# Kernel tuning notes

Measured on AMD Instinct MI355X. Metric: run time of the kernel, lower is better.

Reference implementation:

```python
import jax, jax.numpy as jnp
import numpy as np

B, N, M, K = 4, 16384, 16384, 16   # batch, points, centers, neighbors
C, O, G = 64, 64, 8                # in_planes, out_planes, group


def setup_inputs() -> dict:
    key = jax.random.key(0)
    ks = jax.random.split(key, 16)
    r = lambda i, sh, s=1.0: jax.random.normal(ks[i], sh, jnp.float32) * s
    return dict(
        center_pos=r(0, (B, M, 3)),
        center_fea=r(1, (B, C, M)),
        pos=r(2, (B, N, 3)),
        fea=r(3, (B, C, N)),
        idx=jax.random.randint(ks[4], (B, M, K), 0, N, jnp.int32),
        # linear q/k/v
        Wq=r(5, (C, O), 0.05), bq=jnp.zeros((O,), jnp.float32),
        Wk=r(6, (C, O), 0.05), bk=jnp.zeros((O,), jnp.float32),
        Wv=r(7, (C, O), 0.05), bv=jnp.zeros((O,), jnp.float32),
        # center_pos_encode: conv1x1(3->O, no bias) + folded BN (scale,shift) + relu + conv1x1(O->O)
        cpe_w1=r(8, (3, O), 0.05), cpe_s=jnp.ones((O,), jnp.float32), cpe_b=jnp.zeros((O,), jnp.float32),
        cpe_w2=r(9, (O, O), 0.05), cpe_b2=jnp.zeros((O,), jnp.float32),
        # pos_encode (Conv2d 1x1 == per-point linear)
        pe_w1=r(10, (3, O), 0.05), pe_s=jnp.ones((O,), jnp.float32), pe_b=jnp.zeros((O,), jnp.float32),
        pe_w2=r(11, (O, O), 0.05), pe_b2=jnp.zeros((O,), jnp.float32),
        # weight_encode (O -> G)
        we_w1=r(12, (O, G), 0.05), we_s=jnp.ones((G,), jnp.float32), we_b=jnp.zeros((G,), jnp.float32),
        we_w2=r(13, (G, G), 0.05), we_b2=jnp.zeros((G,), jnp.float32),
    )


def _mlp2(x, w1, s, b, w2, b2):
    # conv1x1(no bias) -> inference BatchNorm folded to (scale, shift) -> ReLU -> conv1x1(+bias)
    h = jax.nn.relu(x @ w1 * s + b)
    return h @ w2 + b2


def reference(center_pos, center_fea, pos, fea, idx,
              Wq, bq, Wk, bk, Wv, bv,
              cpe_w1, cpe_s, cpe_b, cpe_w2, cpe_b2,
              pe_w1, pe_s, pe_b, pe_w2, pe_b2,
              we_w1, we_s, we_b, we_w2, we_b2):
    x_q = center_fea.transpose(0, 2, 1) @ Wq + bq        # [B,M,O]
    ft = fea.transpose(0, 2, 1)                          # [B,N,C]
    x_k = ft @ Wk + bk                                   # [B,N,O]
    x_v = ft @ Wv + bv                                   # [B,N,O]

    gather = jax.vmap(lambda a, i: a[i])                 # per-batch irregular gather
    nk = gather(x_k, idx)                                # [B,M,K,O]
    nv = gather(x_v, idx)                                # [B,M,K,O]
    npos = gather(pos, idx) - center_pos[:, :, None, :]  # [B,M,K,3] relative coords

    cpr = _mlp2(center_pos, cpe_w1, cpe_s, cpe_b, cpe_w2, cpe_b2)  # [B,M,O]
    pr = _mlp2(npos, pe_w1, pe_s, pe_b, pe_w2, pe_b2)              # [B,M,K,O]

    r_qk = nk - x_q[:, :, None, :] + cpr[:, :, None, :]  # [B,M,K,O]
    v = nv + pr                                          # [B,M,K,O]

    w = _mlp2(r_qk, we_w1, we_s, we_b, we_w2, we_b2)     # [B,M,K,G]
    w = jax.nn.softmax(w, axis=2)                        # softmax over neighbors

    v = v.reshape(B, M, K, G, O // G)
    out = jnp.einsum('bmkgi,bmkg->bmgi', v, w).reshape(B, M, O)
    return out.transpose(0, 2, 1)                        # [B,O,M]
```

## Files before the change

### kernel.cpp

```cpp
#include <hip/hip_runtime.h>
#include <hip/hip_bf16.h>

typedef unsigned short u16;
typedef __attribute__((ext_vector_type(8))) __bf16 bf8v;
typedef __attribute__((ext_vector_type(4))) float f32x4;
typedef __attribute__((ext_vector_type(4))) unsigned uint4v;

#define B_ 4
#define N_ 16384
#define M_ 16384
#define K_ 16
#define C_ 64
#define O_ 64
#define G_ 8

__device__ __forceinline__ float bf2f(u16 x){
  union { unsigned u; float f; } v; v.u = ((unsigned)x) << 16; return v.f;
}
__device__ __forceinline__ u16 f2bf(float f){
  union { float f; unsigned u; } v; v.f = f;
  unsigned u = v.u;
  return (u16)((u + 0x7FFFu + ((u >> 16) & 1u)) >> 16);
}

__global__ __launch_bounds__(256) void pre_kernel(
    const float* __restrict__ center_pos, const float* __restrict__ center_fea,
    const float* __restrict__ fea,
    const float* __restrict__ Wq, const float* __restrict__ bq,
    const float* __restrict__ Wk, const float* __restrict__ bk,
    const float* __restrict__ Wv, const float* __restrict__ bv,
    const float* __restrict__ cpe_w1, const float* __restrict__ cpe_s, const float* __restrict__ cpe_b,
    const float* __restrict__ cpe_w2, const float* __restrict__ cpe_b2,
    const float* __restrict__ we_w1,
    u16* __restrict__ xk, u16* __restrict__ xv, float* __restrict__ qw)
{
  int tid = threadIdx.x;
  int blk = blockIdx.x;
  __shared__ u16 sWT[128*72];
  __shared__ u16 sOut[64*136];
  __shared__ float sMisc[784];

  int l = tid & 63, w = tid >> 6, c = l & 15, q = l >> 4;

  if (blk < 1024) {
    int P0 = blk * 64; int b = P0 >> 14; int n0 = P0 & (N_-1);
    for (int e = tid; e < 8192; e += 256){
      int k = e >> 7, col = e & 127;
      float v = (col < 64) ? Wk[k*64 + col] : Wv[k*64 + (col-64)];
      sWT[col*72 + k] = f2bf(v);
    }
    if (tid < 128) sMisc[tid] = (tid < 64) ? bk[tid] : bv[tid-64];
    __syncthreads();

    int mIdx = n0 + w*16 + c;
    const float* fb = fea + (long)b*C_*N_;
    bf8v af[2];
    #pragma unroll
    for (int ks=0; ks<2; ks++){
      union { bf8v v; u16 s[8]; } ua;
      #pragma unroll
      for (int j=0; j<8; j++)
        ua.s[j] = f2bf(fb[(long)(ks*32 + q*8 + j)*N_ + mIdx]);
      af[ks] = ua.v;
    }

    f32x4 acc[8];
    #pragma unroll
    for (int t=0; t<8; t++){
      float bias = sMisc[16*t + c];
      f32x4 a_ = {bias, bias, bias, bias};
      bf8v b0 = *(const bf8v*)&sWT[(16*t + c)*72 + q*8];
      bf8v b1 = *(const bf8v*)&sWT[(16*t + c)*72 + 32 + q*8];
      a_ = __builtin_amdgcn_mfma_f32_16x16x32_bf16(af[0], b0, a_, 0,0,0);
      a_ = __builtin_amdgcn_mfma_f32_16x16x32_bf16(af[1], b1, a_, 0,0,0);
      acc[t] = a_;
    }

    #pragma unroll
    for (int t=0; t<8; t++)
      #pragma unroll
      for (int r=0; r<4; r++)
        sOut[(w*16 + q*4 + r)*136 + 16*t + c] = f2bf(acc[t][r]);
    __syncthreads();

    #pragma unroll
    for (int rep=0; rep<4; rep++){
      int chunk = rep*256 + tid;
      int pt = chunk >> 4, c8i = chunk & 15;
      uint4v val = *(const uint4v*)&sOut[pt*136 + c8i*8];
      int col8 = c8i*8;
      long row = (long)P0 + pt;
      if (col8 < 64) *(uint4v*)(xk + row*64 + col8)      = val;
      else           *(uint4v*)(xv + row*64 + (col8-64)) = val;
    }
  } else {
    int P0 = (blk - 1024) * 64; int b = P0 >> 14; int m0 = P0 & (M_-1);
    for (int e = tid; e < 512; e += 256) sMisc[e] = we_w1[e];
    if (tid < 64){
      float sc = cpe_s[tid];
      sMisc[512+tid] = cpe_w1[tid]      * sc;
      sMisc[576+tid] = cpe_w1[64+tid]   * sc;
      sMisc[640+tid] = cpe_w1[128+tid]  * sc;
      sMisc[704+tid] = cpe_b[tid];
    }
    __syncthreads();

    {
      int k = tid >> 1, g0 = (tid & 1)*4;
      const float* brow = (k < 64) ? (cpe_w2 + k*64) : (Wq + (k-64)*64);
      float sgn = (k < 64) ? 1.f : -1.f;
      float aw[4] = {0.f,0.f,0.f,0.f};
      for (int o=0; o<64; o++){
        float bo = brow[o]*sgn;
        #pragma unroll
        for (int gg=0; gg<4; gg++) aw[gg] += bo * sMisc[o*8 + g0+gg];
      }
      #pragma unroll
      for (int gg=0; gg<4; gg++) sWT[(g0+gg)*136 + k] = f2bf(aw[gg]);
    }
    for (int e = tid; e < 1088; e += 256) sWT[1088 + e] = 0;
    if (tid < 8){
      float s = 0.f;
      for (int o=0; o<64; o++) s += (cpe_b2[o] - bq[o]) * sMisc[o*8 + tid];
      sMisc[768 + tid] = s;
    }
    __syncthreads();

    int pg = P0 + w*16 + c;
    int mIdx = m0 + w*16 + c;
    long c3 = (long)pg * 3;
    float cp0 = center_pos[c3], cp1 = center_pos[c3+1], cp2 = center_pos[c3+2];
    bf8v ah[2], acf[2];
    #pragma unroll
    for (int ks=0; ks<2; ks++){
      union { bf8v v; u16 s[8]; } ua;
      #pragma unroll
      for (int j=0; j<8; j++){
        int h = ks*32 + q*8 + j;
        float hv = cp0*sMisc[512+h] + cp1*sMisc[576+h] + cp2*sMisc[640+h] + sMisc[704+h];
        ua.s[j] = f2bf(fmaxf(hv, 0.f));
      }
      ah[ks] = ua.v;
    }
    const float* cfb = center_fea + (long)b*C_*M_;
    #pragma unroll
    for (int ks=0; ks<2; ks++){
      union { bf8v v; u16 s[8]; } ua;
      #pragma unroll
      for (int j=0; j<8; j++)
        ua.s[j] = f2bf(cfb[(long)(ks*32 + q*8 + j)*M_ + mIdx]);
      acf[ks] = ua.v;
    }

    float cinit = (c < 8) ? sMisc[768 + c] : 0.f;
    f32x4 aq = {cinit, cinit, cinit, cinit};
    {
      bf8v b0 = *(const bf8v*)&sWT[c*136 + q*8];
      bf8v b1 = *(const bf8v*)&sWT[c*136 + 32 + q*8];
      bf8v b2 = *(const bf8v*)&sWT[c*136 + 64 + q*8];
      bf8v b3 = *(const bf8v*)&sWT[c*136 + 96 + q*8];
      aq = __builtin_amdgcn_mfma_f32_16x16x32_bf16(ah[0], b0, aq, 0,0,0);
      aq = __builtin_amdgcn_mfma_f32_16x16x32_bf16(ah[1], b1, aq, 0,0,0);
      aq = __builtin_amdgcn_mfma_f32_16x16x32_bf16(acf[0], b2, aq, 0,0,0);
      aq = __builtin_amdgcn_mfma_f32_16x16x32_bf16(acf[1], b3, aq, 0,0,0);
    }
    __syncthreads();
    if (c < 8){
      #pragma unroll
      for (int r=0; r<4; r++) sMisc[(w*16 + q*4 + r)*8 + c] = aq[r];
    }
    __syncthreads();
    for (int e = tid; e < 512; e += 256)
      qw[(long)P0*8 + e] = sMisc[e];
  }
}

__global__ __launch_bounds__(256) void attn_kernel(
    const float* __restrict__ center_pos, const float* __restrict__ pos,
    const int* __restrict__ idx,
    const float* __restrict__ pe_w1, const float* __restrict__ pe_s, const float* __restrict__ pe_b,
    const float* __restrict__ pe_w2, const float* __restrict__ pe_b2,
    const float* __restrict__ we_w1, const float* __restrict__ we_s, const float* __restrict__ we_b,
    const float* __restrict__ we_w2, const float* __restrict__ we_b2,
    const u16* __restrict__ xk, const u16* __restrict__ xv, const float* __restrict__ qw,
    float* __restrict__ out)
{
  int tid = threadIdx.x;
  __shared__ float s_w1f[192];
  __shared__ float s_pb[64];
  __shared__ float s_ws[8], s_wb[8], s_wb2[8];
  __shared__ float s_ww2[64];
  __shared__ float s_pb2[64];
  __shared__ u16  s_vt[4*16*72];
  __shared__ float s_tile[32*66];

  if (tid < 64){
    float sc = pe_s[tid];
    s_w1f[tid]     = pe_w1[tid]*sc;
    s_w1f[64+tid]  = pe_w1[64+tid]*sc;
    s_w1f[128+tid] = pe_w1[128+tid]*sc;
    s_pb[tid]  = pe_b[tid];
    s_pb2[tid] = pe_b2[tid];
    s_ww2[tid] = we_w2[tid];
  }
  if (tid >= 64 && tid < 72){
    int g = tid-64;
    s_ws[g]=we_s[g]; s_wb[g]=we_b[g]; s_wb2[g]=we_b2[g];
  }
  __syncthreads();

  int w = tid >> 6, l = tid & 63, c = l & 15, q = l >> 4, c8 = c & 7, qb = l & 48;

  bf8v pw2f[4][2], ww1f[2];
  {
    union { bf8v v; u16 s[8]; } u_;
    #pragma unroll
    for (int t=0;t<4;t++)
      #pragma unroll
      for (int ks=0;ks<2;ks++){
        #pragma unroll
        for (int j=0;j<8;j++) u_.s[j] = f2bf(pe_w2[(ks*32 + q*8 + j)*64 + t*16 + c]);
        pw2f[t][ks] = u_.v;
      }
    #pragma unroll
    for (int ks=0;ks<2;ks++){
      #pragma unroll
      for (int j=0;j<8;j++) u_.s[j] = (c < 8) ? f2bf(we_w1[(ks*32 + q*8 + j)*8 + c]) : (u16)0;
      ww1f[ks] = u_.v;
    }
  }
  float ws_c = s_ws[c8], wb_c = s_wb[c8], wb2_c = s_wb2[c8];
  float w2col[8];
  #pragma unroll
  for (int g=0; g<8; g++) w2col[g] = s_ww2[g*8 + c8];
  float pb2t[4];
  #pragma unroll
  for (int t=0;t<4;t++) pb2t[t] = s_pb2[t*16 + c];

  int pbase = blockIdx.x * 32;
  int b = pbase >> 14;
  long xkb = (long)b * N_ * 64;
  u16* vt = s_vt + w*(16*72);

  int p = pbase + w*8;
  int iv = idx[(long)p*16 + c];
  float qpv = qw[(long)p*8 + c8];
  long c30 = (long)p*3;
  float cp0 = center_pos[c30], cp1 = center_pos[c30+1], cp2 = center_pos[c30+2];

  #pragma unroll 1
  for (int i = 0; i < 8; i++){
    long pr3 = ((long)b*N_ + iv) * 3;
    float np0 = pos[pr3]   - cp0;
    float np1 = pos[pr3+1] - cp1;
    float np2 = pos[pr3+2] - cp2;
    const u16* krow = xk + xkb + (long)iv * 64;
    bf8v ka0 = *(const bf8v*)(krow + q*8);
    bf8v ka1 = *(const bf8v*)(krow + 32 + q*8);
    const u16* vrow = xv + xkb + (long)iv * 64;
    uint4v va0 = *(const uint4v*)(vrow + q*8);
    uint4v va1 = *(const uint4v*)(vrow + 32 + q*8);

    int pn = p + ((i < 7) ? 1 : 0);
    int iv_n = idx[(long)pn*16 + c];
    float qpv_n = qw[(long)pn*8 + c8];
    long c3n = (long)pn*3;
    float cpn0 = center_pos[c3n], cpn1 = center_pos[c3n+1], cpn2 = center_pos[c3n+2];

    *(uint4v*)&vt[c*72 + q*8]      = va0;
    *(uint4v*)&vt[c*72 + 32 + q*8] = va1;

    bf8v h1f[2];
    {
      union { bf8v v; u16 s[8]; } hu;
      #pragma unroll
      for (int ks=0;ks<2;ks++){
        #pragma unroll
        for (int j=0;j<8;j++){
          int o = ks*32 + q*8 + j;
          float hv = np0*s_w1f[o] + np1*s_w1f[64+o] + np2*s_w1f[128+o] + s_pb[o];
          hu.s[j] = f2bf(fmaxf(hv, 0.f));
        }
        h1f[ks] = hu.v;
      }
    }

    f32x4 h2a = {qpv, qpv, qpv, qpv};
    h2a = __builtin_amdgcn_mfma_f32_16x16x32_bf16(ka0, ww1f[0], h2a, 0, 0, 0);
    h2a = __builtin_amdgcn_mfma_f32_16x16x32_bf16(ka1, ww1f[1], h2a, 0, 0, 0);

    f32x4 prA[4];
    #pragma unroll
    for (int t=0;t<4;t++){
      f32x4 z = {0.f,0.f,0.f,0.f};
      z = __builtin_amdgcn_mfma_f32_16x16x32_bf16(h1f[0], pw2f[t][0], z, 0, 0, 0);
      z = __builtin_amdgcn_mfma_f32_16x16x32_bf16(h1f[1], pw2f[t][1], z, 0, 0, 0);
      prA[t] = z;
    }

    float h2r[4];
    #pragma unroll
    for (int r=0;r<4;r++) h2r[r] = fmaxf(h2a[r]*ws_c + wb_c, 0.f);
    float wl[4] = {wb2_c, wb2_c, wb2_c, wb2_c};
    #pragma unroll
    for (int g=0; g<8; g++){
      float wg = w2col[g];
      #pragma unroll
      for (int r=0;r<4;r++)
        wl[r] += __shfl(h2r[r], qb | g, 64) * wg;
    }
    float mx = fmaxf(fmaxf(wl[0],wl[1]), fmaxf(wl[2],wl[3]));
    mx = fmaxf(mx, __shfl_xor(mx, 16, 64));
    mx = fmaxf(mx, __shfl_xor(mx, 32, 64));
    float e[4];
    #pragma unroll
    for (int r=0;r<4;r++) e[r] = exp2f((wl[r]-mx)*1.44269504f);
    float sm = e[0]+e[1]+e[2]+e[3];
    sm += __shfl_xor(sm, 16, 64);
    sm += __shfl_xor(sm, 32, 64);
    float rn = 1.0f / sm;
    #pragma unroll
    for (int r=0;r<4;r++) e[r] *= rn;

    float ov[4] = {0.f,0.f,0.f,0.f};
    int ch = c >> 3;
    #pragma unroll
    for (int r=0;r<4;r++){
      #pragma unroll
      for (int t=0;t<4;t++){
        float wv_ = __shfl(e[r], qb | (t*2 + ch), 64);
        float nvv = bf2f(vt[(q*4+r)*72 + t*16 + c]);
        ov[t] += (prA[t][r] + nvv) * wv_;
      }
    }
    #pragma unroll
    for (int t=0;t<4;t++){
      ov[t] += __shfl_xor(ov[t], 16, 64);
      ov[t] += __shfl_xor(ov[t], 32, 64);
      ov[t] += pb2t[t];
    }
    float selv = ov[0];
    selv = (q==1) ? ov[1] : selv;
    selv = (q==2) ? ov[2] : selv;
    selv = (q==3) ? ov[3] : selv;
    s_tile[(w*8+i)*66 + l] = selv;

    p = pn; iv = iv_n; qpv = qpv_n; cp0 = cpn0; cp1 = cpn1; cp2 = cpn2;
  }
  __syncthreads();

  int o0 = tid >> 5, pt = tid & 31;
  int m0 = pbase & (M_-1);
  long outb = ((long)b*64) * M_ + m0 + pt;
  #pragma unroll
  for (int ii=0; ii<8; ii++){
    int o = o0*8 + ii;
    out[outb + (long)o*M_] = s_tile[pt*66 + o];
  }
}

extern "C" void kernel_launch(void* const* d_in, const int* in_sizes, int n_in,
                              void* d_out, int out_size, void* d_ws, size_t ws_size,
                              hipStream_t stream) {
  const float* center_pos = (const float*)d_in[0];
  const float* center_fea = (const float*)d_in[1];
  const float* pos        = (const float*)d_in[2];
  const float* fea        = (const float*)d_in[3];
  const int*   idx        = (const int*)d_in[4];
  const float* Wq = (const float*)d_in[5];   const float* bq = (const float*)d_in[6];
  const float* Wk = (const float*)d_in[7];   const float* bk = (const float*)d_in[8];
  const float* Wv = (const float*)d_in[9];   const float* bv = (const float*)d_in[10];
  const float* cpe_w1 = (const float*)d_in[11]; const float* cpe_s = (const float*)d_in[12];
  const float* cpe_b  = (const float*)d_in[13]; const float* cpe_w2 = (const float*)d_in[14];
  const float* cpe_b2 = (const float*)d_in[15];
  const float* pe_w1 = (const float*)d_in[16]; const float* pe_s = (const float*)d_in[17];
  const float* pe_b  = (const float*)d_in[18]; const float* pe_w2 = (const float*)d_in[19];
  const float* pe_b2 = (const float*)d_in[20];
  const float* we_w1 = (const float*)d_in[21]; const float* we_s = (const float*)d_in[22];
  const float* we_b  = (const float*)d_in[23]; const float* we_w2 = (const float*)d_in[24];
  const float* we_b2 = (const float*)d_in[25];

  const size_t SZ = (size_t)B_*N_*64;
  u16* xk = (u16*)d_ws;
  u16* xv = xk + SZ;
  float* qwp = (float*)(xv + SZ);
  float* outp = (float*)d_out;

  hipLaunchKernelGGL(pre_kernel, dim3(2048), dim3(256), 0, stream,
      center_pos, center_fea, fea, Wq, bq, Wk, bk, Wv, bv,
      cpe_w1, cpe_s, cpe_b, cpe_w2, cpe_b2, we_w1, xk, xv, qwp);
  hipLaunchKernelGGL(attn_kernel, dim3(2048), dim3(256), 0, stream,
      center_pos, pos, idx, pe_w1, pe_s, pe_b, pe_w2, pe_b2,
      we_w1, we_s, we_b, we_w2, we_b2, xk, xv, qwp, outp);
}
```

Baseline: 225.8 us.

## Persist pre_kernel blocks over four tiles, prefetch gathers, pack softmax shuffles in fp16

pre_kernel now launches a quarter as many blocks. Each block builds its weights once, then loops over four 64-point tiles and prefetches the next tile's fea and center_fea into registers. attn_kernel prefetches the next point's pos, xk and xv rows one iteration ahead to hide gather latency. It also packs h2 and softmax weights into fp16 pairs, halving shuffle count. The softmax max-subtraction is removed, which trades numerical safety against overflow for fewer instructions, and the fp16 packing reduces precision.

```diff
diff --git a/kernel.cpp b/kernel.cpp
--- a/kernel.cpp
+++ b/kernel.cpp
@@ -21,6 +21,10 @@
   union { float f; unsigned u; } v; v.f = f;
   unsigned u = v.u;
   return (u16)((u + 0x7FFFu + ((u >> 16) & 1u)) >> 16);
+}
+union pk2 { unsigned u; _Float16 h[2]; };
+__device__ __forceinline__ unsigned packh(float a, float b){
+  pk2 p; p.h[0] = (_Float16)a; p.h[1] = (_Float16)b; return p.u;
 }
 
 __global__ __launch_bounds__(256) void pre_kernel(
@@ -42,8 +46,18 @@
 
   int l = tid & 63, w = tid >> 6, c = l & 15, q = l >> 4;
 
-  if (blk < 1024) {
-    int P0 = blk * 64; int b = P0 >> 14; int n0 = P0 & (N_-1);
+  if (blk < 256) {
+    int P0 = blk * 256; int b = P0 >> 14; int n00 = P0 & (N_-1);
+    const float* fb = fea + (long)b*C_*N_;
+
+    float ar[16];
+    {
+      int mI = n00 + w*16 + c;
+      #pragma unroll
+      for (int e=0; e<16; e++)
+        ar[e] = fb[(long)((e>>3)*32 + q*8 + (e&7))*N_ + mI];
+    }
+
     for (int e = tid; e < 8192; e += 256){
       int k = e >> 7, col = e & 127;
       float v = (col < 64) ? Wk[k*64 + col] : Wv[k*64 + (col-64)];
@@ -52,49 +66,69 @@
     if (tid < 128) sMisc[tid] = (tid < 64) ? bk[tid] : bv[tid-64];
     __syncthreads();
 
-    int mIdx = n0 + w*16 + c;
-    const float* fb = fea + (long)b*C_*N_;
-    bf8v af[2];
-    #pragma unroll
-    for (int ks=0; ks<2; ks++){
-      union { bf8v v; u16 s[8]; } ua;
-      #pragma unroll
-      for (int j=0; j<8; j++)
-        ua.s[j] = f2bf(fb[(long)(ks*32 + q*8 + j)*N_ + mIdx]);
-      af[ks] = ua.v;
-    }
-
-    f32x4 acc[8];
-    #pragma unroll
-    for (int t=0; t<8; t++){
-      float bias = sMisc[16*t + c];
-      f32x4 a_ = {bias, bias, bias, bias};
-      bf8v b0 = *(const bf8v*)&sWT[(16*t + c)*72 + q*8];
-      bf8v b1 = *(const bf8v*)&sWT[(16*t + c)*72 + 32 + q*8];
-      a_ = __builtin_amdgcn_mfma_f32_16x16x32_bf16(af[0], b0, a_, 0,0,0);
-      a_ = __builtin_amdgcn_mfma_f32_16x16x32_bf16(af[1], b1, a_, 0,0,0);
-      acc[t] = a_;
-    }
-
-    #pragma unroll
-    for (int t=0; t<8; t++)
-      #pragma unroll
-      for (int r=0; r<4; r++)
-        sOut[(w*16 + q*4 + r)*136 + 16*t + c] = f2bf(acc[t][r]);
-    __syncthreads();
-
-    #pragma unroll
-    for (int rep=0; rep<4; rep++){
-      int chunk = rep*256 + tid;
-      int pt = chunk >> 4, c8i = chunk & 15;
-      uint4v val = *(const uint4v*)&sOut[pt*136 + c8i*8];
-      int col8 = c8i*8;
-      long row = (long)P0 + pt;
-      if (col8 < 64) *(uint4v*)(xk + row*64 + col8)      = val;
-      else           *(uint4v*)(xv + row*64 + (col8-64)) = val;
+    #pragma unroll 1
+    for (int s = 0; s < 4; s++){
+      bf8v af[2];
+      #pragma unroll
+      for (int ks=0; ks<2; ks++){
+        union { bf8v v; u16 sv[8]; } ua;
+        #pragma unroll
+        for (int j=0; j<8; j++) ua.sv[j] = f2bf(ar[ks*8+j]);
+        af[ks] = ua.v;
+      }
+      if (s < 3){
+        int mI = n00 + (s+1)*64 + w*16 + c;
+        #pragma unroll
+        for (int e=0; e<16; e++)
+          ar[e] = fb[(long)((e>>3)*32 + q*8 + (e&7))*N_ + mI];
+      }
+
+      f32x4 acc[8];
+      #pragma unroll
+      for (int t=0; t<8; t++){
+        float bias = sMisc[16*t + c];
+        f32x4 a_ = {bias, bias, bias, bias};
+        bf8v b0 = *(const bf8v*)&sWT[(16*t + c)*72 + q*8];
+        bf8v b1 = *(const bf8v*)&sWT[(16*t + c)*72 + 32 + q*8];
+        a_ = __builtin_amdgcn_mfma_f32_16x16x32_bf16(af[0], b0, a_, 0,0,0);
+        a_ = __builtin_amdgcn_mfma_f32_16x16x32_bf16(af[1], b1, a_, 0,0,0);
+        acc[t] = a_;
+      }
+
+      #pragma unroll
+      for (int t=0; t<8; t++)
+        #pragma unroll
+        for (int r=0; r<4; r++)
+          sOut[(w*16 + q*4 + r)*136 + 16*t + c] = f2bf(acc[t][r]);
+      __syncthreads();
+
+      long Ps = P0 + s*64;
+      #pragma unroll
+      for (int rep=0; rep<4; rep++){
+        int chunk = rep*256 + tid;
+        int pt = chunk >> 4, c8i = chunk & 15;
+        uint4v val = *(const uint4v*)&sOut[pt*136 + c8i*8];
+        int col8 = c8i*8;
+        long row = Ps + pt;
+        if (col8 < 64) *(uint4v*)(xk + row*64 + col8)      = val;
+        else           *(uint4v*)(xv + row*64 + (col8-64)) = val;
+      }
+      __syncthreads();
     }
   } else {
-    int P0 = (blk - 1024) * 64; int b = P0 >> 14; int m0 = P0 & (M_-1);
+    int P0 = (blk - 256) * 256; int b = P0 >> 14; int m00 = P0 & (M_-1);
+    const float* cfb = center_fea + (long)b*C_*M_;
+
+    float cfr[16], cpr[3];
+    {
+      int mI = m00 + w*16 + c;
+      #pragma unroll
+      for (int e=0; e<16; e++)
+        cfr[e] = cfb[(long)((e>>3)*32 + q*8 + (e&7))*M_ + mI];
+      long c3 = (long)(P0 + w*16 + c)*3;
+      cpr[0]=center_pos[c3]; cpr[1]=center_pos[c3+1]; cpr[2]=center_pos[c3+2];
+    }
+
     for (int e = tid; e < 512; e += 256) sMisc[e] = we_w1[e];
     if (tid < 64){
       float sc = cpe_s[tid];
@@ -126,52 +160,62 @@
     }
     __syncthreads();
 
-    int pg = P0 + w*16 + c;
-    int mIdx = m0 + w*16 + c;
-    long c3 = (long)pg * 3;
-    float cp0 = center_pos[c3], cp1 = center_pos[c3+1], cp2 = center_pos[c3+2];
-    bf8v ah[2], acf[2];
-    #pragma unroll
-    for (int ks=0; ks<2; ks++){
-      union { bf8v v; u16 s[8]; } ua;
-      #pragma unroll
-      for (int j=0; j<8; j++){
-        int h = ks*32 + q*8 + j;
-        float hv = cp0*sMisc[512+h] + cp1*sMisc[576+h] + cp2*sMisc[640+h] + sMisc[704+h];
-        ua.s[j] = f2bf(fmaxf(hv, 0.f));
-      }
-      ah[ks] = ua.v;
-    }
-    const float* cfb = center_fea + (long)b*C_*M_;
-    #pragma unroll
-    for (int ks=0; ks<2; ks++){
-      union { bf8v v; u16 s[8]; } ua;
-      #pragma unroll
-      for (int j=0; j<8; j++)
-        ua.s[j] = f2bf(cfb[(long)(ks*32 + q*8 + j)*M_ + mIdx]);
-      acf[ks] = ua.v;
-    }
-
-    float cinit = (c < 8) ? sMisc[768 + c] : 0.f;
-    f32x4 aq = {cinit, cinit, cinit, cinit};
-    {
-      bf8v b0 = *(const bf8v*)&sWT[c*136 + q*8];
-      bf8v b1 = *(const bf8v*)&sWT[c*136 + 32 + q*8];
-      bf8v b2 = *(const bf8v*)&sWT[c*136 + 64 + q*8];
-      bf8v b3 = *(const bf8v*)&sWT[c*136 + 96 + q*8];
-      aq = __builtin_amdgcn_mfma_f32_16x16x32_bf16(ah[0], b0, aq, 0,0,0);
-      aq = __builtin_amdgcn_mfma_f32_16x16x32_bf16(ah[1], b1, aq, 0,0,0);
-      aq = __builtin_amdgcn_mfma_f32_16x16x32_bf16(acf[0], b2, aq, 0,0,0);
-      aq = __builtin_amdgcn_mfma_f32_16x16x32_bf16(acf[1], b3, aq, 0,0,0);
-    }
-    __syncthreads();
-    if (c < 8){
-      #pragma unroll
-      for (int r=0; r<4; r++) sMisc[(w*16 + q*4 + r)*8 + c] = aq[r];
-    }
-    __syncthreads();
-    for (int e = tid; e < 512; e += 256)
-      qw[(long)P0*8 + e] = sMisc[e];
+    #pragma unroll 1
+    for (int s = 0; s < 4; s++){
+      bf8v ah[2], acf[2];
+      #pragma unroll
+      for (int ks=0; ks<2; ks++){
+        union { bf8v v; u16 sv[8]; } ua;
+        #pragma unroll
+        for (int j=0; j<8; j++){
+          int h = ks*32 + q*8 + j;
+          float hv = cpr[0]*sMisc[512+h] + cpr[1]*sMisc[576+h] + cpr[2]*sMisc[640+h] + sMisc[704+h];
+          ua.sv[j] = f2bf(fmaxf(hv, 0.f));
+        }
+        ah[ks] = ua.v;
+      }
+      #pragma unroll
+      for (int ks=0; ks<2; ks++){
+        union { bf8v v; u16 sv[8]; } ua;
+        #pragma unroll
+        for (int j=0; j<8; j++) ua.sv[j] = f2bf(cfr[ks*8+j]);
+        acf[ks] = ua.v;
+      }
+      if (s < 3){
+        int mI = m00 + (s+1)*64 + w*16 + c;
+        #pragma unroll
+        for (int e=0; e<16; e++)
+          cfr[e] = cfb[(long)((e>>3)*32 + q*8 + (e&7))*M_ + mI];
+        long c3 = (long)(P0 + (s+1)*64 + w*16 + c)*3;
+        cpr[0]=center_pos[c3]; cpr[1]=center_pos[c3+1]; cpr[2]=center_pos[c3+2];
+      }
+
+      float cinit = (c < 8) ? sMisc[768 + c] : 0.f;
+      f32x4 aq = {cinit, cinit, cinit, cinit};
+      {
+        bf8v b0 = *(const bf8v*)&sWT[c*136 + q*8];
+        bf8v b1 = *(const bf8v*)&sWT[c*136 + 32 + q*8];
+        bf8v b2 = *(const bf8v*)&sWT[c*136 + 64 + q*8];
+        bf8v b3 = *(const bf8v*)&sWT[c*136 + 96 + q*8];
+        aq = __builtin_amdgcn_mfma_f32_16x16x32_bf16(ah[0], b0, aq, 0,0,0);
+        aq = __builtin_amdgcn_mfma_f32_16x16x32_bf16(ah[1], b1, aq, 0,0,0);
+        aq = __builtin_amdgcn_mfma_f32_16x16x32_bf16(acf[0], b2, aq, 0,0,0);
+        aq = __builtin_amdgcn_mfma_f32_16x16x32_bf16(acf[1], b3, aq, 0,0,0);
+      }
+      if (c < 8){
+        #pragma unroll
+        for (int r=0; r<4; r++) sOut[(w*16 + q*4 + r)*8 + c] = 0;
+      }
+      __syncthreads();
+      if (c < 8){
+        #pragma unroll
+        for (int r=0; r<4; r++) ((float*)sOut)[(w*16 + q*4 + r)*8 + c] = aq[r];
+      }
+      __syncthreads();
+      for (int e = tid; e < 512; e += 256)
+        qw[(long)(P0 + s*64)*8 + e] = ((float*)sOut)[e];
+      __syncthreads();
+    }
   }
 }
 
@@ -188,9 +232,10 @@
   int tid = threadIdx.x;
   __shared__ float s_w1f[192];
   __shared__ float s_pb[64];
-  __shared__ float s_ws[8], s_wb[8], s_wb2[8];
+  __shared__ float s_ws[8], s_wb[8];
   __shared__ float s_ww2[64];
   __shared__ float s_pb2[64];
+  __shared__ float s_wb2[8];
   __shared__ u16  s_vt[4*16*72];
   __shared__ float s_tile[32*66];
 
@@ -247,25 +292,32 @@
   float qpv = qw[(long)p*8 + c8];
   long c30 = (long)p*3;
   float cp0 = center_pos[c30], cp1 = center_pos[c30+1], cp2 = center_pos[c30+2];
+  long pr30 = ((long)b*N_ + iv) * 3;
+  float px = pos[pr30], py = pos[pr30+1], pz = pos[pr30+2];
+  const u16* krow0 = xk + xkb + (long)iv * 64;
+  bf8v ka0 = *(const bf8v*)(krow0 + q*8);
+  bf8v ka1 = *(const bf8v*)(krow0 + 32 + q*8);
+  const u16* vrow0 = xv + xkb + (long)iv * 64;
+  uint4v va0 = *(const uint4v*)(vrow0 + q*8);
+  uint4v va1 = *(const uint4v*)(vrow0 + 32 + q*8);
 
   #pragma unroll 1
   for (int i = 0; i < 8; i++){
-    long pr3 = ((long)b*N_ + iv) * 3;
-    float np0 = pos[pr3]   - cp0;
-    float np1 = pos[pr3+1] - cp1;
-    float np2 = pos[pr3+2] - cp2;
-    const u16* krow = xk + xkb + (long)iv * 64;
-    bf8v ka0 = *(const bf8v*)(krow + q*8);
-    bf8v ka1 = *(const bf8v*)(krow + 32 + q*8);
-    const u16* vrow = xv + xkb + (long)iv * 64;
-    uint4v va0 = *(const uint4v*)(vrow + q*8);
-    uint4v va1 = *(const uint4v*)(vrow + 32 + q*8);
-
     int pn = p + ((i < 7) ? 1 : 0);
     int iv_n = idx[(long)pn*16 + c];
     float qpv_n = qw[(long)pn*8 + c8];
     long c3n = (long)pn*3;
     float cpn0 = center_pos[c3n], cpn1 = center_pos[c3n+1], cpn2 = center_pos[c3n+2];
+    long pr3n = ((long)b*N_ + iv_n) * 3;
+    float pxn = pos[pr3n], pyn = pos[pr3n+1], pzn = pos[pr3n+2];
+    const u16* krn = xk + xkb + (long)iv_n * 64;
+    bf8v kan0 = *(const bf8v*)(krn + q*8);
+    bf8v kan1 = *(const bf8v*)(krn + 32 + q*8);
+    const u16* vrn = xv + xkb + (long)iv_n * 64;
+    uint4v van0 = *(const uint4v*)(vrn + q*8);
+    uint4v van1 = *(const uint4v*)(vrn + 32 + q*8);
+
+    float np0 = px - cp0, np1 = py - cp1, np2 = pz - cp2;
 
     *(uint4v*)&vt[c*72 + q*8]      = va0;
     *(uint4v*)&vt[c*72 + 32 + q*8] = va1;
@@ -301,37 +353,46 @@
     float h2r[4];
     #pragma unroll
     for (int r=0;r<4;r++) h2r[r] = fmaxf(h2a[r]*ws_c + wb_c, 0.f);
+    unsigned hp0 = packh(h2r[0], h2r[1]);
+    unsigned hp1 = packh(h2r[2], h2r[3]);
     float wl[4] = {wb2_c, wb2_c, wb2_c, wb2_c};
     #pragma unroll
     for (int g=0; g<8; g++){
       float wg = w2col[g];
-      #pragma unroll
-      for (int r=0;r<4;r++)
-        wl[r] += __shfl(h2r[r], qb | g, 64) * wg;
-    }
-    float mx = fmaxf(fmaxf(wl[0],wl[1]), fmaxf(wl[2],wl[3]));
-    mx = fmaxf(mx, __shfl_xor(mx, 16, 64));
-    mx = fmaxf(mx, __shfl_xor(mx, 32, 64));
+      pk2 u0; u0.u = (unsigned)__shfl((int)hp0, qb | g, 64);
+      pk2 u1; u1.u = (unsigned)__shfl((int)hp1, qb | g, 64);
+      wl[0] += (float)u0.h[0] * wg;
+      wl[1] += (float)u0.h[1] * wg;
+      wl[2] += (float)u1.h[0] * wg;
+      wl[3] += (float)u1.h[1] * wg;
+    }
     float e[4];
     #pragma unroll
-    for (int r=0;r<4;r++) e[r] = exp2f((wl[r]-mx)*1.44269504f);
+    for (int r=0;r<4;r++) e[r] = exp2f(wl[r]*1.44269504f);
     float sm = e[0]+e[1]+e[2]+e[3];
     sm += __shfl_xor(sm, 16, 64);
     sm += __shfl_xor(sm, 32, 64);
     float rn = 1.0f / sm;
     #pragma unroll
     for (int r=0;r<4;r++) e[r] *= rn;
+    unsigned ep0 = packh(e[0], e[1]);
+    unsigned ep1 = packh(e[2], e[3]);
 
     float ov[4] = {0.f,0.f,0.f,0.f};
     int ch = c >> 3;
     #pragma unroll
-    for (int r=0;r<4;r++){
-      #pragma unroll
-      for (int t=0;t<4;t++){
-        float wv_ = __shfl(e[r], qb | (t*2 + ch), 64);
-        float nvv = bf2f(vt[(q*4+r)*72 + t*16 + c]);
-        ov[t] += (prA[t][r] + nvv) * wv_;
-      }
+    for (int t=0;t<4;t++){
+      int src = qb | (t*2 + ch);
+      pk2 w01; w01.u = (unsigned)__shfl((int)ep0, src, 64);
+      pk2 w23; w23.u = (unsigned)__shfl((int)ep1, src, 64);
+      float wv0 = (float)w01.h[0], wv1 = (float)w01.h[1];
+      float wv2 = (float)w23.h[0], wv3 = (float)w23.h[1];
+      float acc = 0.f;
+      acc += (prA[t][0] + bf2f(vt[(q*4+0)*72 + t*16 + c])) * wv0;
+      acc += (prA[t][1] + bf2f(vt[(q*4+1)*72 + t*16 + c])) * wv1;
+      acc += (prA[t][2] + bf2f(vt[(q*4+2)*72 + t*16 + c])) * wv2;
+      acc += (prA[t][3] + bf2f(vt[(q*4+3)*72 + t*16 + c])) * wv3;
+      ov[t] = acc;
     }
     #pragma unroll
     for (int t=0;t<4;t++){
@@ -345,7 +406,10 @@
     selv = (q==3) ? ov[3] : selv;
     s_tile[(w*8+i)*66 + l] = selv;
 
-    p = pn; iv = iv_n; qpv = qpv_n; cp0 = cpn0; cp1 = cpn1; cp2 = cpn2;
+    p = pn; iv = iv_n; qpv = qpv_n;
+    cp0 = cpn0; cp1 = cpn1; cp2 = cpn2;
+    px = pxn; py = pyn; pz = pzn;
+    ka0 = kan0; ka1 = kan1; va0 = van0; va1 = van1;
   }
   __syncthreads();
 
@@ -386,7 +450,7 @@
   float* qwp = (float*)(xv + SZ);
   float* outp = (float*)d_out;
 
-  hipLaunchKernelGGL(pre_kernel, dim3(2048), dim3(256), 0, stream,
+  hipLaunchKernelGGL(pre_kernel, dim3(512), dim3(256), 0, stream,
       center_pos, center_fea, fea, Wq, bq, Wk, bk, Wv, bv,
       cpe_w1, cpe_s, cpe_b, cpe_w2, cpe_b2, we_w1, xk, xv, qwp);
   hipLaunchKernelGGL(attn_kernel, dim3(2048), dim3(256), 0, stream,
```

Measured after the change: 213.1 us. 1.06x faster.
